# Kernel optimization log

Hardware: AMD Instinct MI355X
Metric: run time of the kernel (lower is better)

The kernel has to match this reference:

```python
import jax, jax.numpy as jnp
import numpy as np

D = 256
RANK = 64
H = 8
DH = D // H
TOPK = 32  # top-k survivors per query row
NEG = -1e9


def lowrank(x, u, v):
    # x:[...,d] @ u:[d,rank] @ v:[rank,d]
    return (x @ u) @ v


def setup_inputs() -> dict:
    key = jax.random.key(0)
    ks = jax.random.split(key, 13)
    s_u = 1.0 / np.sqrt(D)
    s_v = 1.0 / np.sqrt(RANK)

    def pu(k):
        return jax.random.normal(k, (D, RANK), jnp.float32) * s_u

    def pv(k):
        return jax.random.normal(k, (RANK, D), jnp.float32) * s_v

    return {
        "x": jax.random.normal(ks[0], (2, 2048, D), jnp.float32),
        "ne_u": pu(ks[1]), "ne_v": pv(ks[2]),
        "wq_u": pu(ks[3]), "wq_v": pv(ks[4]),
        "wk_u": pu(ks[5]), "wk_v": pv(ks[6]),
        "wv_u": pu(ks[7]), "wv_v": pv(ks[8]),
        "wo_u": pu(ks[9]), "wo_v": pv(ks[10]),
        "es_u": pu(ks[11]), "es_v": pv(ks[12]),
    }


def reference(x, ne_u, ne_v, wq_u, wq_v, wk_u, wk_v, wv_u, wv_v, wo_u, wo_v, es_u, es_v):
    B, N, _ = x.shape
    # node embedding (low-rank projection)
    h = lowrank(x, ne_u, ne_v)  # [B,N,d]

    # low-rank multi-head Q/K/V
    def heads(t):  # [B,N,d] -> [B,H,N,dh]
        return t.reshape(B, N, H, DH).transpose(0, 2, 1, 3)

    q = heads(lowrank(h, wq_u, wq_v))
    k = heads(lowrank(h, wk_u, wk_v))
    v = heads(lowrank(h, wv_u, wv_v))

    scores = jnp.einsum("bhnd,bhmd->bhnm", q, k) / jnp.sqrt(jnp.float32(DH))
    # top-k sparsification per query row
    kth = jax.lax.top_k(scores, TOPK)[0][..., -1:]  # [B,H,N,1]
    masked = jnp.where(scores >= kth, scores, NEG)
    attn = jax.nn.softmax(masked, axis=-1)  # [B,H,N,N]

    out = jnp.einsum("bhnm,bhmd->bhnd", attn, v)  # [B,H,N,dh]
    out = out.transpose(0, 2, 1, 3).reshape(B, N, D)
    h2 = lowrank(out, wo_u, wo_v)  # output projection

    # edge scores -> adjacency with sigmoid + zero diagonal epilogue
    el = lowrank(h2, es_u, es_v)  # [B,N,d]
    adjacency = jax.nn.sigmoid(jnp.einsum("bnd,bmd->bnm", el, el))
    adjacency = adjacency * (1.0 - jnp.eye(N, dtype=adjacency.dtype))
    return adjacency, attn
```

## Files before the change

kernel.cpp:

```cpp
#include <hip/hip_runtime.h>
#include <hip/hip_bf16.h>
#include <cstdint>
#include <cstddef>

#define ATTN_OFF (2u*2048u*2048u)
#define SLOTS 48
#define DELTA 1e-3f
#define MAXB 16
#define CCAP 96

typedef __attribute__((ext_vector_type(8))) short bf16x8;
typedef __attribute__((ext_vector_type(4))) float f32x4;

__device__ __forceinline__ unsigned short bf16_hi(float f) {
  __hip_bfloat16 h = __float2bfloat16(f);
  return *(unsigned short*)&h;
}
__device__ __forceinline__ float bf16_val(unsigned short u) {
  __hip_bfloat16 h = *(__hip_bfloat16*)&u;
  return __bfloat162float(h);
}

__global__ __launch_bounds__(256) void fused_qkv_kernel(
    const float* __restrict__ x, const float* __restrict__ ne_u,
    const float* __restrict__ ne_v, const float* __restrict__ wq_u,
    const float* __restrict__ wq_v, const float* __restrict__ wk_u,
    const float* __restrict__ wk_v, const float* __restrict__ wv_u,
    const float* __restrict__ wv_v, double* __restrict__ qd,
    double* __restrict__ kd, unsigned short* __restrict__ qh,
    unsigned short* __restrict__ ql, unsigned short* __restrict__ kh,
    unsigned short* __restrict__ kl, float* __restrict__ v) {
  __shared__ double xm[4][64];
  __shared__ double hrow[4][256];
  __shared__ double mid2[4][64];

  int tid = threadIdx.x;
  int rr = tid >> 6;
  int j  = tid & 63;
  int row = blockIdx.x * 4 + rr;
  int b = row >> 11, m = row & 2047;
  const double INV = 0.17677669529663688110021109052621;

  const float* xr = x + (size_t)row * 256;
  {
    double a0 = 0, a1 = 0, a2 = 0, a3 = 0;
#pragma unroll 8
    for (int k4 = 0; k4 < 64; ++k4) {
      int kk = k4 * 4;
      a0 = fma((double)xr[kk + 0], (double)ne_u[(kk + 0) * 64 + j], a0);
      a1 = fma((double)xr[kk + 1], (double)ne_u[(kk + 1) * 64 + j], a1);
      a2 = fma((double)xr[kk + 2], (double)ne_u[(kk + 2) * 64 + j], a2);
      a3 = fma((double)xr[kk + 3], (double)ne_u[(kk + 3) * 64 + j], a3);
    }
    xm[rr][j] = (a0 + a1) + (a2 + a3);
  }
  __syncthreads();

#pragma unroll
  for (int cc = 0; cc < 4; ++cc) {
    int col = j + 64 * cc;
    double o0 = 0, o1 = 0, o2 = 0, o3 = 0;
#pragma unroll 4
    for (int r4 = 0; r4 < 16; ++r4) {
      int r = r4 * 4;
      o0 = fma(xm[rr][r + 0], (double)ne_v[(r + 0) * 256 + col], o0);
      o1 = fma(xm[rr][r + 1], (double)ne_v[(r + 1) * 256 + col], o1);
      o2 = fma(xm[rr][r + 2], (double)ne_v[(r + 2) * 256 + col], o2);
      o3 = fma(xm[rr][r + 3], (double)ne_v[(r + 3) * 256 + col], o3);
    }
    hrow[rr][col] = (o0 + o1) + (o2 + o3);
  }
  __syncthreads();

  for (int p = 0; p < 3; ++p) {
    const float* pu = (p == 0) ? wq_u : (p == 1) ? wk_u : wv_u;
    const float* pw = (p == 0) ? wq_v : (p == 1) ? wk_v : wv_v;

    double a0 = 0, a1 = 0, a2 = 0, a3 = 0;
#pragma unroll 8
    for (int k4 = 0; k4 < 64; ++k4) {
      int kk = k4 * 4;
      a0 = fma(hrow[rr][kk + 0], (double)pu[(kk + 0) * 64 + j], a0);
      a1 = fma(hrow[rr][kk + 1], (double)pu[(kk + 1) * 64 + j], a1);
      a2 = fma(hrow[rr][kk + 2], (double)pu[(kk + 2) * 64 + j], a2);
      a3 = fma(hrow[rr][kk + 3], (double)pu[(kk + 3) * 64 + j], a3);
    }
    mid2[rr][j] = (a0 + a1) + (a2 + a3);
    __syncthreads();

#pragma unroll
    for (int cc = 0; cc < 4; ++cc) {
      int col = j + 64 * cc;
      double o0 = 0, o1 = 0, o2 = 0, o3 = 0;
#pragma unroll 4
      for (int r4 = 0; r4 < 16; ++r4) {
        int r = r4 * 4;
        o0 = fma(mid2[rr][r + 0], (double)pw[(r + 0) * 256 + col], o0);
        o1 = fma(mid2[rr][r + 1], (double)pw[(r + 1) * 256 + col], o1);
        o2 = fma(mid2[rr][r + 2], (double)pw[(r + 2) * 256 + col], o2);
        o3 = fma(mid2[rr][r + 3], (double)pw[(r + 3) * 256 + col], o3);
      }
      double o = (o0 + o1) + (o2 + o3);
      if (p == 2) {
        v[(size_t)row * 256 + col] = (float)o;
      } else {
        int hh = col >> 5, d = col & 31;
        size_t haddr = (((size_t)(b * 8 + hh)) * 2048 + m) * 32 + d;
        if (p == 0) {
          qd[(size_t)row * 256 + col] = o;
          float f = (float)(o * INV);
          unsigned short hi = bf16_hi(f);
          float lof = f - bf16_val(hi);
          qh[haddr] = hi;
          ql[haddr] = bf16_hi(lof);
        } else {
          kd[(size_t)row * 256 + col] = o;
          float f = (float)o;
          unsigned short hi = bf16_hi(f);
          float lof = f - bf16_val(hi);
          kh[haddr] = hi;
          kl[haddr] = bf16_hi(lof);
        }
      }
    }
    __syncthreads();
  }
}

template <typename InT, int MODE>
__global__ __launch_bounds__(256) void lowrank_kernel(
    const InT* __restrict__ in, const float* __restrict__ u,
    const float* __restrict__ vw, void* __restrict__ out0,
    void* __restrict__ out1, void* __restrict__ out2) {
  __shared__ double mid[4][64];
  int tid = threadIdx.x;
  int rr = tid >> 6;
  int j  = tid & 63;
  int row = blockIdx.x * 4 + rr;

  const InT* inr = in + (size_t)row * 256;
  double a0 = 0, a1 = 0, a2 = 0, a3 = 0;
#pragma unroll 8
  for (int k4 = 0; k4 < 64; ++k4) {
    int kk = k4 * 4;
    a0 = fma((double)inr[kk + 0], (double)u[(kk + 0) * 64 + j], a0);
    a1 = fma((double)inr[kk + 1], (double)u[(kk + 1) * 64 + j], a1);
    a2 = fma((double)inr[kk + 2], (double)u[(kk + 2) * 64 + j], a2);
    a3 = fma((double)inr[kk + 3], (double)u[(kk + 3) * 64 + j], a3);
  }
  mid[rr][j] = (a0 + a1) + (a2 + a3);
  __syncthreads();

#pragma unroll
  for (int cc = 0; cc < 4; ++cc) {
    int col = j + 64 * cc;
    double o0 = 0, o1 = 0, o2 = 0, o3 = 0;
#pragma unroll 4
    for (int r4 = 0; r4 < 16; ++r4) {
      int r = r4 * 4;
      o0 = fma(mid[rr][r + 0], (double)vw[(r + 0) * 256 + col], o0);
      o1 = fma(mid[rr][r + 1], (double)vw[(r + 1) * 256 + col], o1);
      o2 = fma(mid[rr][r + 2], (double)vw[(r + 2) * 256 + col], o2);
      o3 = fma(mid[rr][r + 3], (double)vw[(r + 3) * 256 + col], o3);
    }
    double o = (o0 + o1) + (o2 + o3);
    if constexpr (MODE == 1) {
      ((float*)out0)[(size_t)row * 256 + col] = (float)o;
    } else {
      float f = (float)o;
      unsigned short hi = bf16_hi(f);
      float lof = f - bf16_val(hi);
      ((unsigned short*)out1)[(size_t)row * 256 + col] = hi;
      ((unsigned short*)out2)[(size_t)row * 256 + col] = bf16_hi(lof);
    }
  }
}

__global__ __launch_bounds__(512, 4) void attn_kernel(
    const unsigned short* __restrict__ qh, const unsigned short* __restrict__ ql,
    const unsigned short* __restrict__ kh, const unsigned short* __restrict__ kl,
    const double* __restrict__ qd, const double* __restrict__ kd,
    float* __restrict__ attn, float* __restrict__ pval,
    unsigned short* __restrict__ pidx) {
  __shared__ unsigned hist[16][256];
  __shared__ float cand[16][CCAP];
  __shared__ float rowmax_s[16][8];
  __shared__ float zpart_s[16][8];
  __shared__ float mx_s[16];
  __shared__ float kth_s[16];
  __shared__ float zinv_s[16];
  __shared__ int   kB_s[16];
  __shared__ unsigned kneed_s[16];
  __shared__ unsigned ccnt[16];
  __shared__ unsigned scnt[16];
  __shared__ unsigned chi_s[16];
  __shared__ unsigned bcnt[16];
  __shared__ unsigned short bidx[16][MAXB];
  __shared__ unsigned short bkeep[16][MAXB];
  __shared__ double bs64[16][MAXB];

  int tid = threadIdx.x;
  int bx  = blockIdx.x;
  int slab = bx >> 7;
  int rowtile = bx & 127;
  int b = slab >> 3, hh = slab & 7;
  int w = tid >> 6;
  int l = tid & 63;
  int g = l >> 4;
  int li = l & 15;
  const double INV64 = 0.17677669529663688110021109052621;

  size_t qoff = (((size_t)slab * 2048 + rowtile * 16 + li) * 32) + g * 8;
  bf16x8 a_hi = *(const bf16x8*)(qh + qoff);
  bf16x8 a_lo = *(const bf16x8*)(ql + qoff);

  float s[16][4];
  size_t kbase = ((size_t)slab * 2048 + w * 256 + li) * 32 + g * 8;
#pragma unroll
  for (int tt = 0; tt < 16; ++tt) {
    bf16x8 b_hi = *(const bf16x8*)(kh + kbase + (size_t)tt * 512);
    bf16x8 b_lo = *(const bf16x8*)(kl + kbase + (size_t)tt * 512);
    f32x4 acc = {0.f, 0.f, 0.f, 0.f};
    acc = __builtin_amdgcn_mfma_f32_16x16x32_bf16(a_hi, b_hi, acc, 0, 0, 0);
    acc = __builtin_amdgcn_mfma_f32_16x16x32_bf16(a_hi, b_lo, acc, 0, 0, 0);
    acc = __builtin_amdgcn_mfma_f32_16x16x32_bf16(a_lo, b_hi, acc, 0, 0, 0);
#pragma unroll
    for (int reg = 0; reg < 4; ++reg) s[tt][reg] = acc[reg];
  }

  for (int i = tid; i < 16 * 256; i += 512) ((unsigned*)hist)[i] = 0u;
  if (tid < 16) {
    ccnt[tid] = 0u; scnt[tid] = 0u; chi_s[tid] = 0u; bcnt[tid] = 0u;
    kth_s[tid] = -1e30f; kB_s[tid] = -1;
  }
  size_t prow0 = ((size_t)slab * 2048 + rowtile * 16);
  for (int i = tid; i < 16 * SLOTS; i += 512) {
    pval[prow0 * SLOTS + i] = 0.0f;
    pidx[prow0 * SLOTS + i] = 0;
  }
  {
    float lmx[4];
#pragma unroll
    for (int reg = 0; reg < 4; ++reg) {
      float m = s[0][reg];
#pragma unroll
      for (int tt = 1; tt < 16; ++tt) m = fmaxf(m, s[tt][reg]);
      lmx[reg] = m;
    }
#pragma unroll
    for (int off = 1; off < 16; off <<= 1) {
#pragma unroll
      for (int reg = 0; reg < 4; ++reg)
        lmx[reg] = fmaxf(lmx[reg], __shfl_xor(lmx[reg], (unsigned)off, 16));
    }
    if (li == 0) {
#pragma unroll
      for (int reg = 0; reg < 4; ++reg) rowmax_s[4 * g + reg][w] = lmx[reg];
    }
  }
  __syncthreads();

  if (tid < 16) {
    float m = rowmax_s[tid][0];
#pragma unroll
    for (int i = 1; i < 8; ++i) m = fmaxf(m, rowmax_s[tid][i]);
    mx_s[tid] = m;
  }
  __syncthreads();

#pragma unroll
  for (int reg = 0; reg < 4; ++reg) {
    int rloc = 4 * g + reg;
    float mx = mx_s[rloc];
#pragma unroll
    for (int tt = 0; tt < 16; ++tt) {
      int bb = (int)((mx - s[tt][reg]) * 16.0f);
      bb = bb > 255 ? 255 : bb;
      atomicAdd(&hist[rloc][bb], 1u);
    }
  }
  __syncthreads();

  if (w < 4) {
    int rloc = w * 4 + g;
    unsigned cnt16 = 0;
#pragma unroll
    for (int i = 0; i < 16; ++i) cnt16 += hist[rloc][li * 16 + i];
    unsigned pre = cnt16;
#pragma unroll
    for (int off = 1; off < 16; off <<= 1) {
      unsigned t = __shfl_up(pre, (unsigned)off, 16);
      if (li >= off) pre += t;
    }
    unsigned excl = pre - cnt16;
    bool flag = (excl < 32u) && (pre >= 32u);
    unsigned long long bal = __ballot(flag);
    unsigned seg = (unsigned)((bal >> (g * 16)) & 0xFFFFull);
    if (flag) {
      int src = __ffs(seg) - 1;
      if (li == src) {
        unsigned cum = excl;
        int B = 255; unsigned cb = 0;
#pragma unroll
        for (int i = 0; i < 16; ++i) {
          unsigned hv = hist[rloc][li * 16 + i];
          if (cum < 32u && cum + hv >= 32u) { B = li * 16 + i; cb = cum; }
          cum += hv;
        }
        kB_s[rloc] = B;
        kneed_s[rloc] = 32u - cb;
      }
    }
  }
  __syncthreads();

#pragma unroll
  for (int reg = 0; reg < 4; ++reg) {
    int rloc = 4 * g + reg;
    float mx = mx_s[rloc];
    int kB = kB_s[rloc];
#pragma unroll
    for (int tt = 0; tt < 16; ++tt) {
      int bb = (int)((mx - s[tt][reg]) * 16.0f);
      bb = bb > 255 ? 255 : bb;
      if (bb == kB) {
        unsigned slot = atomicAdd(&ccnt[rloc], 1u);
        if (slot < (unsigned)CCAP) cand[rloc][slot] = s[tt][reg];
      }
    }
  }
  __syncthreads();

  if (w < 4) {
    int rloc = w * 4 + g;
    unsigned n0 = ccnt[rloc];
    n0 = n0 > (unsigned)CCAP ? (unsigned)CCAP : n0;
    unsigned need = kneed_s[rloc];
    if (need > n0) need = n0;
    for (unsigned ci = (unsigned)li; ci < n0; ci += 16u) {
      float x = cand[rloc][ci];
      unsigned r = 0;
      for (unsigned jj = 0; jj < n0; ++jj) {
        float y = cand[rloc][jj];
        r += (y > x || (y == x && jj < ci)) ? 1u : 0u;
      }
      if (r == need - 1u) kth_s[rloc] = x;
    }
  }
  __syncthreads();

#pragma unroll
  for (int reg = 0; reg < 4; ++reg) {
    int rloc = 4 * g + reg;
    float kth = kth_s[rloc];
    unsigned cnt = 0;
#pragma unroll
    for (int tt = 0; tt < 16; ++tt) {
      float v = s[tt][reg];
      if (v > kth + DELTA) {
        ++cnt;
      } else if (!(v < kth - DELTA)) {
        unsigned slot = atomicAdd(&bcnt[rloc], 1u);
        if (slot < (unsigned)MAXB)
          bidx[rloc][slot] = (unsigned short)(w * 256 + tt * 16 + li);
      }
    }
#pragma unroll
    for (int off = 1; off < 16; off <<= 1)
      cnt += (unsigned)__shfl_xor((int)cnt, off, 16);
    if (li == 0) atomicAdd(&chi_s[rloc], cnt);
  }
  __syncthreads();

  if (w < 4) {
    int rloc = w * 4 + g;
    unsigned bn = bcnt[rloc];
    bn = bn > (unsigned)MAXB ? (unsigned)MAXB : bn;
    const double* qrow =
        qd + ((size_t)(b * 2048 + rowtile * 16 + rloc)) * 256 + hh * 32;
    for (unsigned ci = (unsigned)li; ci < bn; ci += 16u) {
      int m = bidx[rloc][ci];
      const double* krow = kd + ((size_t)(b * 2048 + m)) * 256 + hh * 32;
      double acc = 0.0;
#pragma unroll 8
      for (int d = 0; d < 32; ++d) acc = fma(qrow[d], krow[d], acc);
      bs64[rloc][ci] = acc * INV64;
    }
    unsigned need2 = 32u - chi_s[rloc];
    for (unsigned ci = (unsigned)li; ci < bn; ci += 16u) {
      double x = bs64[rloc][ci];
      unsigned r = 0;
      for (unsigned jj = 0; jj < bn; ++jj)
        r += (bs64[rloc][jj] > x) ? 1u : 0u;
      bkeep[rloc][ci] = (r < need2) ? 1 : 0;
    }
  }
  __syncthreads();

  {
    float zs[4];
#pragma unroll
    for (int reg = 0; reg < 4; ++reg) {
      int rloc = 4 * g + reg;
      float mx = mx_s[rloc], kth = kth_s[rloc];
      unsigned bn = bcnt[rloc];
      bn = bn > (unsigned)MAXB ? (unsigned)MAXB : bn;
      float z = 0.0f;
#pragma unroll
      for (int tt = 0; tt < 16; ++tt) {
        float v = s[tt][reg];
        bool keep;
        if (v > kth + DELTA) {
          keep = true;
        } else if (v < kth - DELTA) {
          keep = false;
        } else {
          unsigned short col = (unsigned short)(w * 256 + tt * 16 + li);
          keep = (v >= kth);
          for (unsigned jj = 0; jj < bn; ++jj) {
            if (bidx[rloc][jj] == col) { keep = bkeep[rloc][jj] != 0; break; }
          }
        }
        float p = keep ? __expf(v - mx) : 0.0f;
        s[tt][reg] = p;
        z += p;
      }
      zs[reg] = z;
    }
#pragma unroll
    for (int off = 1; off < 16; off <<= 1) {
#pragma unroll
      for (int reg = 0; reg < 4; ++reg)
        zs[reg] += __shfl_xor(zs[reg], (unsigned)off, 16);
    }
    if (li == 0) {
#pragma unroll
      for (int reg = 0; reg < 4; ++reg) zpart_s[4 * g + reg][w] = zs[reg];
    }
  }
  __syncthreads();

  if (tid < 16) {
    float z = 0.0f;
#pragma unroll
    for (int i = 0; i < 8; ++i) z += zpart_s[tid][i];
    zinv_s[tid] = 1.0f / z;
  }
  __syncthreads();

#pragma unroll
  for (int reg = 0; reg < 4; ++reg) {
    int rloc = 4 * g + reg;
    float rz = zinv_s[rloc];
    float* pr = attn + (prow0 + rloc) * 2048 + w * 256 + li;
    float* pvr = pval + (prow0 + rloc) * SLOTS;
    unsigned short* pir = pidx + (prow0 + rloc) * SLOTS;
#pragma unroll
    for (int tt = 0; tt < 16; ++tt) {
      float p = s[tt][reg];
      float pn = p * rz;
      pr[tt * 16] = pn;
      if (p > 0.0f) {
        unsigned slot = atomicAdd(&scnt[rloc], 1u);
        if (slot < (unsigned)SLOTS) {
          pvr[slot] = pn;
          pir[slot] = (unsigned short)(w * 256 + tt * 16 + li);
        }
      }
    }
  }
}

__global__ __launch_bounds__(256) void pv_sparse_kernel(
    const float* __restrict__ pval, const unsigned short* __restrict__ pidx,
    const float* __restrict__ v, float* __restrict__ out) {
  __shared__ float vals[8][SLOTS];
  __shared__ unsigned short idxs[8][SLOTS];
  int tid = threadIdx.x;
  int grp = blockIdx.x;
  int slab = grp >> 8;
  int rg = grp & 255;
  int b = slab >> 3, hh = slab & 7;
  int r = tid >> 5, dh = tid & 31;

  for (int e = tid; e < 8 * SLOTS; e += 256) {
    int rr = e / SLOTS, ii = e % SLOTS;
    size_t base = ((size_t)slab * 2048 + rg * 8 + rr) * SLOTS + ii;
    vals[rr][ii] = pval[base];
    idxs[rr][ii] = pidx[base];
  }
  __syncthreads();

  const float* vb = v + (size_t)b * 2048 * 256 + hh * 32 + dh;
  float acc = 0.0f;
#pragma unroll 4
  for (int i = 0; i < SLOTS; ++i) {
    float p = vals[r][i];
    int m = idxs[r][i];
    acc = fmaf(p, vb[(size_t)m * 256], acc);
  }
  int n = rg * 8 + r;
  out[((size_t)(b * 2048 + n)) * 256 + hh * 32 + dh] = acc;
}

__global__ __launch_bounds__(256) void adj_mfma_kernel(
    const unsigned short* __restrict__ elh, const unsigned short* __restrict__ ell,
    float* __restrict__ adj) {
  int tid = threadIdx.x;
  int l = tid & 63, w = tid >> 6;
  int li = l & 15, g = l >> 4;
  int b = blockIdx.z, rt = blockIdx.y, ct = blockIdx.x;

  int arow = rt * 64 + w * 16 + li;
  size_t abase = ((size_t)(b * 2048 + arow)) * 256 + g * 8;
  size_t bbase = ((size_t)(b * 2048 + ct * 64 + li)) * 256 + g * 8;

  f32x4 acc0 = {0.f, 0.f, 0.f, 0.f};
  f32x4 acc1 = {0.f, 0.f, 0.f, 0.f};
  f32x4 acc2 = {0.f, 0.f, 0.f, 0.f};
  f32x4 acc3 = {0.f, 0.f, 0.f, 0.f};

#pragma unroll
  for (int kc = 0; kc < 8; ++kc) {
    bf16x8 a_hi = *(const bf16x8*)(elh + abase + kc * 32);
    bf16x8 a_lo = *(const bf16x8*)(ell + abase + kc * 32);
#pragma unroll
    for (int t = 0; t < 4; ++t) {
      bf16x8 b_hi = *(const bf16x8*)(elh + bbase + (size_t)t * 16 * 256 + kc * 32);
      bf16x8 b_lo = *(const bf16x8*)(ell + bbase + (size_t)t * 16 * 256 + kc * 32);
      f32x4* pa = (t == 0) ? &acc0 : (t == 1) ? &acc1 : (t == 2) ? &acc2 : &acc3;
      *pa = __builtin_amdgcn_mfma_f32_16x16x32_bf16(a_hi, b_hi, *pa, 0, 0, 0);
      *pa = __builtin_amdgcn_mfma_f32_16x16x32_bf16(a_hi, b_lo, *pa, 0, 0, 0);
      *pa = __builtin_amdgcn_mfma_f32_16x16x32_bf16(a_lo, b_hi, *pa, 0, 0, 0);
    }
  }

  int orow0 = rt * 64 + w * 16 + g * 4;
#pragma unroll
  for (int t = 0; t < 4; ++t) {
    f32x4 a = (t == 0) ? acc0 : (t == 1) ? acc1 : (t == 2) ? acc2 : acc3;
    int cg = ct * 64 + t * 16 + li;
#pragma unroll
    for (int i = 0; i < 4; ++i) {
      int rg = orow0 + i;
      float sg = 1.0f / (1.0f + __expf(-a[i]));
      if (rg == cg) sg = 0.0f;
      adj[((size_t)b * 2048 + rg) * 2048 + cg] = sg;
    }
  }
}

extern "C" void kernel_launch(void* const* d_in, const int* in_sizes, int n_in,
                              void* d_out, int out_size, void* d_ws,
                              size_t ws_size, hipStream_t stream) {
  const float* x    = (const float*)d_in[0];
  const float* ne_u = (const float*)d_in[1];
  const float* ne_v = (const float*)d_in[2];
  const float* wq_u = (const float*)d_in[3];
  const float* wq_v = (const float*)d_in[4];
  const float* wk_u = (const float*)d_in[5];
  const float* wk_v = (const float*)d_in[6];
  const float* wv_u = (const float*)d_in[7];
  const float* wv_v = (const float*)d_in[8];
  const float* wo_u = (const float*)d_in[9];
  const float* wo_v = (const float*)d_in[10];
  const float* es_u = (const float*)d_in[11];
  const float* es_v = (const float*)d_in[12];

  float* adj  = (float*)d_out;
  float* attn = adj + (size_t)ATTN_OFF;

  char* ws = (char*)d_ws;
  double* qd = (double*)(ws);
  double* kd = (double*)(ws + ((size_t)8  << 20));
  unsigned short* qh = (unsigned short*)(ws + ((size_t)16 << 20));
  unsigned short* ql = (unsigned short*)(ws + ((size_t)18 << 20));
  unsigned short* kh = (unsigned short*)(ws + ((size_t)20 << 20));
  unsigned short* kl = (unsigned short*)(ws + ((size_t)22 << 20));
  float* v    = (float*)(ws + ((size_t)24 << 20));
  float* pval = (float*)(ws + ((size_t)28 << 20));
  unsigned short* pidx = (unsigned short*)(ws + ((size_t)35 << 20));
  float* out  = (float*)(ws);
  float* h2   = (float*)(ws + ((size_t)4  << 20));
  unsigned short* elh = (unsigned short*)(ws + ((size_t)8  << 20));
  unsigned short* ell = (unsigned short*)(ws + ((size_t)10 << 20));

  fused_qkv_kernel<<<1024, 256, 0, stream>>>(
      x, ne_u, ne_v, wq_u, wq_v, wk_u, wk_v, wv_u, wv_v,
      qd, kd, qh, ql, kh, kl, v);

  attn_kernel<<<2048, 512, 0, stream>>>(qh, ql, kh, kl, qd, kd, attn, pval, pidx);
  pv_sparse_kernel<<<4096, 256, 0, stream>>>(pval, pidx, v, out);

  lowrank_kernel<float, 1><<<1024, 256, 0, stream>>>(out, wo_u, wo_v, h2, nullptr, nullptr);
  lowrank_kernel<float, 4><<<1024, 256, 0, stream>>>(h2, es_u, es_v, nullptr, elh, ell);

  adj_mfma_kernel<<<dim3(32, 32, 2), 256, 0, stream>>>(elh, ell, adj);
}
```

Measured before the change: 417.7 us.

## Split dense attn writeout into expand kernel and fuse PV with output/edge projections

The attention kernel stops writing the full dense attn matrix and only emits the sparse top-k values and indices. A new expand kernel zero-fills attn rows with nontemporal vector stores and scatters the surviving probabilities into them. The sparse PV product, the wo low-rank projection and the es low-rank projection (with the bf16 hi/lo split) are fused into one kernel that keeps intermediates in shared memory, and these projections now use fp32 instead of fp64. This removes two launches and the global round trips for out and h2, at the cost of fewer blocks (512) in the fused kernel and lower projection precision.

```diff
diff --git a/kernel.cpp b/kernel.cpp
--- a/kernel.cpp
+++ b/kernel.cpp
@@ -127,61 +127,11 @@
   }
 }
 
-template <typename InT, int MODE>
-__global__ __launch_bounds__(256) void lowrank_kernel(
-    const InT* __restrict__ in, const float* __restrict__ u,
-    const float* __restrict__ vw, void* __restrict__ out0,
-    void* __restrict__ out1, void* __restrict__ out2) {
-  __shared__ double mid[4][64];
-  int tid = threadIdx.x;
-  int rr = tid >> 6;
-  int j  = tid & 63;
-  int row = blockIdx.x * 4 + rr;
-
-  const InT* inr = in + (size_t)row * 256;
-  double a0 = 0, a1 = 0, a2 = 0, a3 = 0;
-#pragma unroll 8
-  for (int k4 = 0; k4 < 64; ++k4) {
-    int kk = k4 * 4;
-    a0 = fma((double)inr[kk + 0], (double)u[(kk + 0) * 64 + j], a0);
-    a1 = fma((double)inr[kk + 1], (double)u[(kk + 1) * 64 + j], a1);
-    a2 = fma((double)inr[kk + 2], (double)u[(kk + 2) * 64 + j], a2);
-    a3 = fma((double)inr[kk + 3], (double)u[(kk + 3) * 64 + j], a3);
-  }
-  mid[rr][j] = (a0 + a1) + (a2 + a3);
-  __syncthreads();
-
-#pragma unroll
-  for (int cc = 0; cc < 4; ++cc) {
-    int col = j + 64 * cc;
-    double o0 = 0, o1 = 0, o2 = 0, o3 = 0;
-#pragma unroll 4
-    for (int r4 = 0; r4 < 16; ++r4) {
-      int r = r4 * 4;
-      o0 = fma(mid[rr][r + 0], (double)vw[(r + 0) * 256 + col], o0);
-      o1 = fma(mid[rr][r + 1], (double)vw[(r + 1) * 256 + col], o1);
-      o2 = fma(mid[rr][r + 2], (double)vw[(r + 2) * 256 + col], o2);
-      o3 = fma(mid[rr][r + 3], (double)vw[(r + 3) * 256 + col], o3);
-    }
-    double o = (o0 + o1) + (o2 + o3);
-    if constexpr (MODE == 1) {
-      ((float*)out0)[(size_t)row * 256 + col] = (float)o;
-    } else {
-      float f = (float)o;
-      unsigned short hi = bf16_hi(f);
-      float lof = f - bf16_val(hi);
-      ((unsigned short*)out1)[(size_t)row * 256 + col] = hi;
-      ((unsigned short*)out2)[(size_t)row * 256 + col] = bf16_hi(lof);
-    }
-  }
-}
-
 __global__ __launch_bounds__(512, 4) void attn_kernel(
     const unsigned short* __restrict__ qh, const unsigned short* __restrict__ ql,
     const unsigned short* __restrict__ kh, const unsigned short* __restrict__ kl,
     const double* __restrict__ qd, const double* __restrict__ kd,
-    float* __restrict__ attn, float* __restrict__ pval,
-    unsigned short* __restrict__ pidx) {
+    float* __restrict__ pval, unsigned short* __restrict__ pidx) {
   __shared__ unsigned hist[16][256];
   __shared__ float cand[16][CCAP];
   __shared__ float rowmax_s[16][8];
@@ -452,18 +402,15 @@
   for (int reg = 0; reg < 4; ++reg) {
     int rloc = 4 * g + reg;
     float rz = zinv_s[rloc];
-    float* pr = attn + (prow0 + rloc) * 2048 + w * 256 + li;
     float* pvr = pval + (prow0 + rloc) * SLOTS;
     unsigned short* pir = pidx + (prow0 + rloc) * SLOTS;
 #pragma unroll
     for (int tt = 0; tt < 16; ++tt) {
       float p = s[tt][reg];
-      float pn = p * rz;
-      pr[tt * 16] = pn;
       if (p > 0.0f) {
         unsigned slot = atomicAdd(&scnt[rloc], 1u);
         if (slot < (unsigned)SLOTS) {
-          pvr[slot] = pn;
+          pvr[slot] = p * rz;
           pir[slot] = (unsigned short)(w * 256 + tt * 16 + li);
         }
       }
@@ -471,36 +418,142 @@
   }
 }
 
-__global__ __launch_bounds__(256) void pv_sparse_kernel(
+__global__ __launch_bounds__(256) void expand_kernel(
     const float* __restrict__ pval, const unsigned short* __restrict__ pidx,
-    const float* __restrict__ v, float* __restrict__ out) {
-  __shared__ float vals[8][SLOTS];
-  __shared__ unsigned short idxs[8][SLOTS];
+    float* __restrict__ attn) {
   int tid = threadIdx.x;
-  int grp = blockIdx.x;
-  int slab = grp >> 8;
-  int rg = grp & 255;
-  int b = slab >> 3, hh = slab & 7;
-  int r = tid >> 5, dh = tid & 31;
-
-  for (int e = tid; e < 8 * SLOTS; e += 256) {
+  size_t row0 = (size_t)blockIdx.x * 16;
+  float* base = attn + row0 * 2048;
+
+  f32x4 z4 = {0.f, 0.f, 0.f, 0.f};
+#pragma unroll
+  for (int it = 0; it < 32; ++it) {
+    int e = tid + 256 * it;
+    __builtin_nontemporal_store(z4, ((f32x4*)base) + e);
+  }
+  __syncthreads();
+
+  for (int e = tid; e < 16 * SLOTS; e += 256) {
     int rr = e / SLOTS, ii = e % SLOTS;
-    size_t base = ((size_t)slab * 2048 + rg * 8 + rr) * SLOTS + ii;
-    vals[rr][ii] = pval[base];
-    idxs[rr][ii] = pidx[base];
-  }
-  __syncthreads();
-
-  const float* vb = v + (size_t)b * 2048 * 256 + hh * 32 + dh;
-  float acc = 0.0f;
+    float p = pval[(row0 + rr) * SLOTS + ii];
+    if (p != 0.0f)
+      base[(size_t)rr * 2048 + pidx[(row0 + rr) * SLOTS + ii]] = p;
+  }
+}
+
+__global__ __launch_bounds__(256) void pv_wo_es_kernel(
+    const float* __restrict__ pval, const unsigned short* __restrict__ pidx,
+    const float* __restrict__ v,
+    const float* __restrict__ wo_u, const float* __restrict__ wo_v,
+    const float* __restrict__ es_u, const float* __restrict__ es_v,
+    unsigned short* __restrict__ elh, unsigned short* __restrict__ ell) {
+  __shared__ float svals[8][8][SLOTS];
+  __shared__ unsigned short sidx[8][8][SLOTS];
+  __shared__ float outr[8][256];
+  __shared__ float mid[8][64];
+  __shared__ float h2r[8][256];
+
+  int tid = threadIdx.x;
+  int bb = blockIdx.x >> 8;
+  int rg = blockIdx.x & 255;
+  int n0 = rg * 8;
+
+  for (int e = tid; e < 8 * 8 * SLOTS; e += 256) {
+    int rr = e / (8 * SLOTS);
+    int rem = e % (8 * SLOTS);
+    int hh = rem / SLOTS, ii = rem % SLOTS;
+    size_t srow = ((size_t)(bb * 8 + hh) * 2048 + n0 + rr) * SLOTS + ii;
+    svals[rr][hh][ii] = pval[srow];
+    sidx[rr][hh][ii] = pidx[srow];
+  }
+  __syncthreads();
+
+  {
+    int d = tid, hh = d >> 5;
+    const float* vb = v + (size_t)bb * 2048 * 256 + d;
+    for (int r = 0; r < 8; ++r) {
+      float acc = 0.f;
 #pragma unroll 4
-  for (int i = 0; i < SLOTS; ++i) {
-    float p = vals[r][i];
-    int m = idxs[r][i];
-    acc = fmaf(p, vb[(size_t)m * 256], acc);
-  }
-  int n = rg * 8 + r;
-  out[((size_t)(b * 2048 + n)) * 256 + hh * 32 + dh] = acc;
+      for (int i = 0; i < SLOTS; ++i) {
+        float p = svals[r][hh][i];
+        int m = sidx[r][hh][i];
+        acc = fmaf(p, vb[(size_t)m * 256], acc);
+      }
+      outr[r][d] = acc;
+    }
+  }
+  __syncthreads();
+
+  {
+    int j = tid & 63, rb = tid >> 6;
+    for (int r = rb; r < 8; r += 4) {
+      float a0 = 0, a1 = 0, a2 = 0, a3 = 0;
+#pragma unroll 8
+      for (int k4 = 0; k4 < 64; ++k4) {
+        int k = k4 * 4;
+        a0 = fmaf(outr[r][k + 0], wo_u[(k + 0) * 64 + j], a0);
+        a1 = fmaf(outr[r][k + 1], wo_u[(k + 1) * 64 + j], a1);
+        a2 = fmaf(outr[r][k + 2], wo_u[(k + 2) * 64 + j], a2);
+        a3 = fmaf(outr[r][k + 3], wo_u[(k + 3) * 64 + j], a3);
+      }
+      mid[r][j] = (a0 + a1) + (a2 + a3);
+    }
+  }
+  __syncthreads();
+
+  {
+    int c = tid;
+    for (int r = 0; r < 8; ++r) {
+      float a0 = 0, a1 = 0, a2 = 0, a3 = 0;
+#pragma unroll 4
+      for (int k4 = 0; k4 < 16; ++k4) {
+        int k = k4 * 4;
+        a0 = fmaf(mid[r][k + 0], wo_v[(k + 0) * 256 + c], a0);
+        a1 = fmaf(mid[r][k + 1], wo_v[(k + 1) * 256 + c], a1);
+        a2 = fmaf(mid[r][k + 2], wo_v[(k + 2) * 256 + c], a2);
+        a3 = fmaf(mid[r][k + 3], wo_v[(k + 3) * 256 + c], a3);
+      }
+      h2r[r][c] = (a0 + a1) + (a2 + a3);
+    }
+  }
+  __syncthreads();
+
+  {
+    int j = tid & 63, rb = tid >> 6;
+    for (int r = rb; r < 8; r += 4) {
+      float a0 = 0, a1 = 0, a2 = 0, a3 = 0;
+#pragma unroll 8
+      for (int k4 = 0; k4 < 64; ++k4) {
+        int k = k4 * 4;
+        a0 = fmaf(h2r[r][k + 0], es_u[(k + 0) * 64 + j], a0);
+        a1 = fmaf(h2r[r][k + 1], es_u[(k + 1) * 64 + j], a1);
+        a2 = fmaf(h2r[r][k + 2], es_u[(k + 2) * 64 + j], a2);
+        a3 = fmaf(h2r[r][k + 3], es_u[(k + 3) * 64 + j], a3);
+      }
+      mid[r][j] = (a0 + a1) + (a2 + a3);
+    }
+  }
+  __syncthreads();
+
+  {
+    int c = tid;
+    for (int r = 0; r < 8; ++r) {
+      float a0 = 0, a1 = 0, a2 = 0, a3 = 0;
+#pragma unroll 4
+      for (int k4 = 0; k4 < 16; ++k4) {
+        int k = k4 * 4;
+        a0 = fmaf(mid[r][k + 0], es_v[(k + 0) * 256 + c], a0);
+        a1 = fmaf(mid[r][k + 1], es_v[(k + 1) * 256 + c], a1);
+        a2 = fmaf(mid[r][k + 2], es_v[(k + 2) * 256 + c], a2);
+        a3 = fmaf(mid[r][k + 3], es_v[(k + 3) * 256 + c], a3);
+      }
+      float o = (a0 + a1) + (a2 + a3);
+      size_t addr = ((size_t)(bb * 2048 + n0 + r)) * 256 + c;
+      unsigned short hi = bf16_hi(o);
+      elh[addr] = hi;
+      ell[addr] = bf16_hi(o - bf16_val(hi));
+    }
+  }
 }
 
 __global__ __launch_bounds__(256) void adj_mfma_kernel(
@@ -580,8 +633,6 @@
   float* v    = (float*)(ws + ((size_t)24 << 20));
   float* pval = (float*)(ws + ((size_t)28 << 20));
   unsigned short* pidx = (unsigned short*)(ws + ((size_t)35 << 20));
-  float* out  = (float*)(ws);
-  float* h2   = (float*)(ws + ((size_t)4  << 20));
   unsigned short* elh = (unsigned short*)(ws + ((size_t)8  << 20));
   unsigned short* ell = (unsigned short*)(ws + ((size_t)10 << 20));
 
@@ -589,11 +640,10 @@
       x, ne_u, ne_v, wq_u, wq_v, wk_u, wk_v, wv_u, wv_v,
       qd, kd, qh, ql, kh, kl, v);
 
-  attn_kernel<<<2048, 512, 0, stream>>>(qh, ql, kh, kl, qd, kd, attn, pval, pidx);
-  pv_sparse_kernel<<<4096, 256, 0, stream>>>(pval, pidx, v, out);
-
-  lowrank_kernel<float, 1><<<1024, 256, 0, stream>>>(out, wo_u, wo_v, h2, nullptr, nullptr);
-  lowrank_kernel<float, 4><<<1024, 256, 0, stream>>>(h2, es_u, es_v, nullptr, elh, ell);
+  attn_kernel<<<2048, 512, 0, stream>>>(qh, ql, kh, kl, qd, kd, pval, pidx);
+  expand_kernel<<<2048, 256, 0, stream>>>(pval, pidx, attn);
+  pv_wo_es_kernel<<<512, 256, 0, stream>>>(pval, pidx, v, wo_u, wo_v,
+                                           es_u, es_v, elh, ell);
 
   adj_mfma_kernel<<<dim3(32, 32, 2), 256, 0, stream>>>(elh, ell, adj);
 }
```

Measured after the change: 447.4 us. 1.07x slower.
